# Kernel optimization log

Measured on AMD Instinct MI355X. Metric: run time of the kernel, lower is better.

## Reference

```python
import jax, jax.numpy as jnp
import numpy as np

V, E, H, L, T, B, K = 50000, 256, 512, 2, 256, 64, 32


def setup_inputs() -> dict:
    key = jax.random.key(0)
    ks = iter(jax.random.split(key, 64))
    def p(shape, scale=0.05):
        return jax.random.normal(next(ks), shape, jnp.float32) * scale
    inp = {"sentences": jax.random.randint(next(ks), (T, B), 0, V)}
    inp["emb"] = p((V, E), 0.1)
    in_sizes = [E, 2 * H]
    for l in range(L):
        for d in ("f", "r"):
            inp[f"w_ih_l{l}{d}"] = p((4 * H, in_sizes[l]))
            inp[f"w_hh_l{l}{d}"] = p((4 * H, H))
            inp[f"b_ih_l{l}{d}"] = p((4 * H,))
            inp[f"b_hh_l{l}{d}"] = p((4 * H,))
    inp["W_out"] = p((K, 2 * H))
    inp["b_out"] = p((K,))
    inp["transitions"] = p((K, K), 0.1)
    inp["start_trans"] = p((K,), 0.1)
    inp["stop_trans"] = p((K,), 0.1)
    return inp


def _lstm_dir(x, w_ih, w_hh, b_ih, b_hh, reverse):
    # x: (T, B, D). PyTorch gate order: i, f, g, o.
    Hd = w_hh.shape[1]
    xp = jnp.einsum('tbd,gd->tbg', x, w_ih) + b_ih + b_hh  # precompute input proj
    def step(carry, xt):
        h, c = carry
        g = xt + h @ w_hh.T
        i, f, gg, o = jnp.split(g, 4, axis=-1)
        c = jax.nn.sigmoid(f) * c + jax.nn.sigmoid(i) * jnp.tanh(gg)
        h = jax.nn.sigmoid(o) * jnp.tanh(c)
        return (h, c), h
    z = jnp.zeros((x.shape[1], Hd), x.dtype)
    _, hs = jax.lax.scan(step, (z, z), xp, reverse=reverse)
    return hs


def _forward(sentences, emb, layer_params, W_out, b_out, transitions, start_trans, stop_trans):
    x = emb[sentences]  # (T, B, E); dropout is identity at inference
    for (pf, pr) in layer_params:
        hf = _lstm_dir(x, *pf, reverse=False)
        hr = _lstm_dir(x, *pr, reverse=True)
        x = jnp.concatenate([hf, hr], axis=-1)  # (T, B, 2H)
    feats = jnp.einsum('tbh,kh->tbk', x, W_out) + b_out  # (T, B, K)

    # Viterbi: R[b, j, k] = transitions[j, k] + dp[b, k] + feat[b, j]
    dp0 = start_trans + feats[0]
    def vstep(dp, feat):
        R = transitions[None] + dp[:, None, :] + feat[:, :, None]
        return R.max(-1), R.argmax(-1)
    dp, bps = jax.lax.scan(vstep, dp0, feats[1:])  # bps: (T-1, B, K)
    dp = dp + stop_trans
    scores = dp.max(-1)
    last = dp.argmax(-1)
    def back(tag, bp_t):
        prev = jnp.take_along_axis(bp_t, tag[:, None], axis=1)[:, 0]
        return prev, prev
    _, pre = jax.lax.scan(back, last, bps, reverse=True)  # (T-1, B), in time order
    paths = jnp.concatenate([pre, last[None]], axis=0)  # (T, B)
    return scores, paths


def reference(sentences, emb,
              w_ih_l0f, w_hh_l0f, b_ih_l0f, b_hh_l0f,
              w_ih_l0r, w_hh_l0r, b_ih_l0r, b_hh_l0r,
              w_ih_l1f, w_hh_l1f, b_ih_l1f, b_hh_l1f,
              w_ih_l1r, w_hh_l1r, b_ih_l1r, b_hh_l1r,
              W_out, b_out, transitions, start_trans, stop_trans):
    layer_params = [
        ((w_ih_l0f, w_hh_l0f, b_ih_l0f, b_hh_l0f), (w_ih_l0r, w_hh_l0r, b_ih_l0r, b_hh_l0r)),
        ((w_ih_l1f, w_hh_l1f, b_ih_l1f, b_hh_l1f), (w_ih_l1r, w_hh_l1r, b_ih_l1r, b_hh_l1r)),
    ]
    return _forward(sentences, emb, layer_params, W_out, b_out, transitions, start_trans, stop_trans)
```

## Files before the change

### kernel.cpp

```cpp
#include <hip/hip_runtime.h>
#include <cstdint>
#include <cstddef>

#define T_ 256
#define B_ 64
#define E_ 256
#define H_ 512
#define NTAG 32
#define CHK 32
#define HSLOT 33

static constexpr size_t OX1  = 0;
static constexpr size_t SX1  = (size_t)T_*256*B_*4;
static constexpr size_t OX2  = OX1 + SX1;
static constexpr size_t SX2  = SX1;
static constexpr size_t OX0  = OX2;
static constexpr size_t OXP  = OX2 + SX2;
static constexpr size_t SXPC = (size_t)CHK*2048*B_;
static constexpr size_t SXP  = 2*SXPC;
static constexpr size_t OWHH0 = OXP + SXP;
static constexpr size_t SWHH  = (size_t)2*512*512*4;
static constexpr size_t OWHH1 = OWHH0 + SWHH;
static constexpr size_t OWIH0 = OWHH1 + SWHH;
static constexpr size_t SWIH0 = (size_t)2*2048*256;
static constexpr size_t OWIH1 = OWIH0 + SWIH0;
static constexpr size_t SWIH1 = (size_t)2*2048*1024;
static constexpr size_t OWOUT = OWIH1 + SWIH1;
static constexpr size_t SWOUT = (size_t)1024*32;
static constexpr size_t OHH   = OWOUT + SWOUT;
static constexpr size_t SHHL  = (size_t)2*HSLOT*32768;
static constexpr size_t SHH   = 2*SHHL;
static constexpr size_t OCB   = OHH + SHH;
static constexpr size_t SCB   = (size_t)2*2*512*64;
static constexpr size_t OBAR  = OCB + SCB;
static constexpr size_t SBAR  = (size_t)2*2*128*16;
static constexpr size_t OFE   = OBAR + SBAR;
static constexpr size_t SFE   = (size_t)T_*B_*NTAG;
static constexpr size_t OBP   = OFE + SFE;
static constexpr size_t SBP   = (size_t)T_*B_*NTAG/4;
static constexpr size_t WS_FLOATS = OBP + SBP;

__device__ __forceinline__ float sigf(float x){ return 1.0f/(1.0f + expf(-x)); }

__global__ void pack_whh(const float* __restrict__ w, float* __restrict__ out){
  int id = blockIdx.x*256 + threadIdx.x;
  int gate = id & 3, k = (id>>2) & 511, u = id >> 11;
  out[id] = w[((size_t)gate*512 + u)*512 + k];
}
__global__ void pack_wih(const float* __restrict__ w, float* __restrict__ out, int K, int kshift){
  int id = blockIdx.x*256 + threadIdx.x;
  int k = id & (K-1); int jj = (id>>kshift)&15; int g = id>>(kshift+4);
  out[((size_t)g*K + k)*16 + jj] = w[(size_t)(g*16+jj)*K + k];
}
__global__ void pack_wout(const float* __restrict__ w, float* __restrict__ out){
  int id = blockIdx.x*256 + threadIdx.x;
  int k = id & 1023, jj = id>>10;
  out[k*32 + jj] = w[id];
}

__global__ void gather_emb(const int* __restrict__ sent, const float* __restrict__ emb,
                           float* __restrict__ x0){
  int t = blockIdx.x; int lane = threadIdx.x & 63; int w = threadIdx.x >> 6;
  int s = sent[t*B_ + lane];
  const float4* er = (const float4*)emb + (size_t)s*(E_/4);
  float4* xo = (float4*)x0 + (size_t)t*64*64;
  #pragma unroll
  for (int q=0; q<16; ++q){
    int e4 = w*16 + q;
    xo[e4*64 + lane] = er[e4];
  }
}

__global__ __launch_bounds__(256) void proj_kernel(
    const float* __restrict__ xin, const float* __restrict__ wpack,
    const float* __restrict__ bihf, const float* __restrict__ bhhf,
    const float* __restrict__ bihr, const float* __restrict__ bhhr,
    float* __restrict__ xp, int K, int t0){
  int jg = blockIdx.x, i = blockIdx.y, dir = blockIdx.z;
  int t = dir ? (T_-1 - (t0 + i)) : (t0 + i);
  int lane = threadIdx.x & 63;
  int w = __builtin_amdgcn_readfirstlane((int)threadIdx.x) >> 6;
  int kq = K >> 2;
  int n4 = kq >> 2;
  int k40 = (w*kq) >> 2;
  const float4* xi = (const float4*)xin + (size_t)t*(K>>2)*64;
  size_t pstride = (size_t)K*16;
  const float* wp = wpack + (size_t)dir*2048*K + (size_t)(jg*2)*pstride + (size_t)w*kq*16;
  float acc[2][16];
  #pragma unroll
  for (int p=0;p<2;p++)
    #pragma unroll
    for (int jj=0;jj<16;jj++) acc[p][jj] = 0.f;
  for (int k4=0; k4<n4; ++k4){
    float4 h = xi[(k40+k4)*64 + lane];
    float hv[4] = {h.x, h.y, h.z, h.w};
    #pragma unroll
    for (int p=0;p<2;p++){
      const float* wv = wp + p*pstride + k4*64;
      #pragma unroll
      for (int ii=0;ii<4;ii++)
        #pragma unroll
        for (int jj=0;jj<16;jj++)
          acc[p][jj] = fmaf(wv[ii*16+jj], hv[ii], acc[p][jj]);
    }
  }
  __shared__ float red[4][32][64];
  #pragma unroll
  for (int p=0;p<2;p++)
    #pragma unroll
    for (int jj=0;jj<16;jj++) red[w][p*16+jj][lane] = acc[p][jj];
  __syncthreads();
  const float* b1 = dir ? bihr : bihf;
  const float* b2 = dir ? bhhr : bhhf;
  float* xpd = xp + (size_t)dir*SXPC + (size_t)i*2048*64;
  #pragma unroll
  for (int q=0;q<8;q++){
    int rr = w*8 + q;
    float v = red[0][rr][lane] + red[1][rr][lane] + red[2][rr][lane] + red[3][rr][lane];
    int row = jg*32 + rr;
    v += b1[row] + b2[row];
    xpd[(size_t)row*64 + lane] = v;
  }
}

__global__ __launch_bounds__(256,1) void rec_kernel(
    const float* __restrict__ xp, const float* __restrict__ whh,
    float* __restrict__ xout, float* __restrict__ hh, float* __restrict__ cb0,
    int* __restrict__ flags, int step0, int nsteps){
  int bid = blockIdx.x;
  int dir = bid & 1, g = bid >> 1;
  int lane = threadIdx.x & 63;
  int w = __builtin_amdgcn_readfirstlane((int)threadIdx.x >> 6);
  const float* xpd = xp + (size_t)dir*SXPC;
  const float* wbase = whh + (size_t)dir*1048576 + (size_t)g*4*2048;
  float* hhd = hh + (size_t)dir*((size_t)HSLOT*32768);
  float* cb = cb0 + dir*32768;
  int* fl = flags + dir*(128*16);
  __shared__ float red[4][16][64];
  __shared__ float hlds[256];
  int uo = g*4 + w;
  float c = cb[uo*64 + lane];
  size_t xb = ((size_t)uo)*64 + lane;
  float x0v = xpd[xb], x1v = xpd[xb+32768], x2v = xpd[xb+65536], x3v = xpd[xb+98304];
  for (int s=0; s<nsteps; ++s){
    int gstep = step0 + s;
    int t = dir ? (T_-1-gstep) : gstep;
    const float4* hp = (const float4*)(hhd + (size_t)(gstep % HSLOT)*32768);
    float4 hreg[32];
    #pragma unroll
    for (int i=0;i<32;i++) hreg[i] = hp[(w*32+i)*64 + lane];
    float acc[4][4];
    #pragma unroll
    for (int cu=0;cu<4;cu++)
      #pragma unroll
      for (int gt=0;gt<4;gt++) acc[cu][gt]=0.f;
    #pragma unroll
    for (int i=0;i<32;i++){
      float hv[4] = {hreg[i].x, hreg[i].y, hreg[i].z, hreg[i].w};
      #pragma unroll
      for (int cu=0; cu<4; cu++){
        const float4* wr = (const float4*)(wbase + (size_t)cu*2048 + (size_t)(w*128 + i*4)*4);
        #pragma unroll
        for (int kk=0;kk<4;kk++){
          float4 w4 = wr[kk];
          acc[cu][0] = fmaf(w4.x, hv[kk], acc[cu][0]);
          acc[cu][1] = fmaf(w4.y, hv[kk], acc[cu][1]);
          acc[cu][2] = fmaf(w4.z, hv[kk], acc[cu][2]);
          acc[cu][3] = fmaf(w4.w, hv[kk], acc[cu][3]);
        }
      }
    }
    #pragma unroll
    for (int cu=0;cu<4;cu++)
      #pragma unroll
      for (int gt=0;gt<4;gt++) red[w][cu*4+gt][lane] = acc[cu][gt];
    __syncthreads();
    float gv[4];
    #pragma unroll
    for (int gt=0;gt<4;gt++)
      gv[gt] = red[0][w*4+gt][lane] + red[1][w*4+gt][lane]
             + red[2][w*4+gt][lane] + red[3][w*4+gt][lane];
    gv[0] += x0v; gv[1] += x1v; gv[2] += x2v; gv[3] += x3v;
    float iv = sigf(gv[0]), fv = sigf(gv[1]);
    float gg = tanhf(gv[2]), ov = sigf(gv[3]);
    c = fv*c + iv*gg;
    float h = ov*tanhf(c);
    hlds[lane*4 + w] = h;
    __syncthreads();
    if (w == 0){
      float4 hv4 = ((const float4*)hlds)[lane];
      union { float4 f; unsigned long long q[2]; } uu; uu.f = hv4;
      unsigned long long* dst = (unsigned long long*)
          (hhd + (size_t)((gstep+1) % HSLOT)*32768 + (size_t)g*256 + (size_t)lane*4);
      __hip_atomic_store(dst+0, uu.q[0], __ATOMIC_RELAXED, __HIP_MEMORY_SCOPE_AGENT);
      __hip_atomic_store(dst+1, uu.q[1], __ATOMIC_RELAXED, __HIP_MEMORY_SCOPE_AGENT);
    } else if (w == 1){
      float4 hv4 = ((const float4*)hlds)[lane];
      float4* xo = (float4*)(xout + (size_t)t*65536 + (size_t)(dir*128 + g)*256);
      xo[lane] = hv4;
    }
    if (s < nsteps-1){
      if (w == 0){
        asm volatile("s_waitcnt vmcnt(0)" ::: "memory");
      }
      __syncthreads();
      if (threadIdx.x == 0)
        __hip_atomic_store(&fl[g*16], gstep+1, __ATOMIC_RELAXED, __HIP_MEMORY_SCOPE_AGENT);
      size_t xb2 = ((size_t)(s+1)*2048 + uo)*64 + lane;
      x0v = xpd[xb2]; x1v = xpd[xb2+32768]; x2v = xpd[xb2+65536]; x3v = xpd[xb2+98304];
      int tid = threadIdx.x;
      if (tid < 128){
        int target = gstep+1;
        int spins = 0;
        while (__hip_atomic_load(&fl[tid*16], __ATOMIC_RELAXED, __HIP_MEMORY_SCOPE_AGENT) < target){
          __builtin_amdgcn_s_sleep(1);
          if (++spins > (1<<22)) break;
        }
      }
      __syncthreads();
      asm volatile("" ::: "memory");
    }
  }
  cb[uo*64 + lane] = c;
}

__global__ __launch_bounds__(256) void feats_kernel(
    const float* __restrict__ x2, const float* __restrict__ wout,
    const float* __restrict__ bout, float* __restrict__ feats){
  int t = blockIdx.x; int lane = threadIdx.x & 63;
  int w = __builtin_amdgcn_readfirstlane((int)threadIdx.x) >> 6;
  const float4* xi = (const float4*)x2 + (size_t)t*16384;
  const float* wp = wout + (size_t)w*256*32;
  float acc[32];
  #pragma unroll
  for (int j=0;j<32;j++) acc[j] = 0.f;
  for (int k4=0;k4<64;k4++){
    float4 h = xi[(w*64 + k4)*64 + lane];
    float hv[4] = {h.x, h.y, h.z, h.w};
    const float* wv = wp + k4*128;
    #pragma unroll
    for (int ii=0;ii<4;ii++)
      #pragma unroll
      for (int j=0;j<32;j++)
        acc[j] = fmaf(wv[ii*32+j], hv[ii], acc[j]);
  }
  __shared__ float red[4][32][64];
  #pragma unroll
  for (int j=0;j<32;j++) red[w][j][lane] = acc[j];
  __syncthreads();
  __shared__ float tr[64*33];
  #pragma unroll
  for (int q=0;q<8;q++){
    int j = w*8 + q;
    float v = red[0][j][lane]+red[1][j][lane]+red[2][j][lane]+red[3][j][lane] + bout[j];
    tr[lane*33 + j] = v;
  }
  __syncthreads();
  float* fo = feats + (size_t)t*2048;
  int tid = threadIdx.x;
  #pragma unroll
  for (int q=0;q<8;q++){
    int idx = tid*8 + q;
    fo[idx] = tr[(idx>>5)*33 + (idx&31)];
  }
}

__global__ __launch_bounds__(64) void viterbi_kernel(
    const float* __restrict__ feats, const float* __restrict__ trans,
    const float* __restrict__ start, const float* __restrict__ stop,
    unsigned char* __restrict__ bp, float* __restrict__ out){
  int lane = threadIdx.x & 63;
  int b = blockIdx.x*2 + (lane>>5);
  int j = lane & 31;
  int base = lane & 32;
  float tr[32];
  #pragma unroll
  for (int k=0;k<32;k++) tr[k] = trans[j*32+k];
  float dp = start[j] + feats[b*32 + j];
  for (int t=1;t<T_;t++){
    float best = __shfl(dp, base, 64) + tr[0];
    int arg = 0;
    #pragma unroll
    for (int k=1;k<32;k++){
      float v = __shfl(dp, base + k, 64) + tr[k];
      if (v > best){ best = v; arg = k; }
    }
    dp = best + feats[((size_t)t*64 + b)*32 + j];
    bp[(size_t)(t-1)*2048 + b*32 + j] = (unsigned char)arg;
  }
  dp += stop[j];
  float bv = dp; int bi = j;
  #pragma unroll
  for (int off=1; off<32; off<<=1){
    float ov = __shfl_xor(bv, off, 64);
    int oi   = __shfl_xor(bi, off, 64);
    if (ov > bv || (ov == bv && oi < bi)){ bv = ov; bi = oi; }
  }
  if (j == 0){
    out[b] = bv;
    int cur = bi;
    out[64 + 255*64 + b] = (float)cur;
    for (int t=254;t>=0;t--){
      cur = bp[(size_t)t*2048 + b*32 + cur];
      out[64 + t*64 + b] = (float)cur;
    }
  }
}

extern "C" void kernel_launch(void* const* d_in, const int* in_sizes, int n_in,
                              void* d_out, int out_size, void* d_ws, size_t ws_size,
                              hipStream_t stream){
  const int*   sent      = (const int*)  d_in[0];
  const float* emb       = (const float*)d_in[1];
  const float* w_ih_l0f  = (const float*)d_in[2];
  const float* w_hh_l0f  = (const float*)d_in[3];
  const float* b_ih_l0f  = (const float*)d_in[4];
  const float* b_hh_l0f  = (const float*)d_in[5];
  const float* w_ih_l0r  = (const float*)d_in[6];
  const float* w_hh_l0r  = (const float*)d_in[7];
  const float* b_ih_l0r  = (const float*)d_in[8];
  const float* b_hh_l0r  = (const float*)d_in[9];
  const float* w_ih_l1f  = (const float*)d_in[10];
  const float* w_hh_l1f  = (const float*)d_in[11];
  const float* b_ih_l1f  = (const float*)d_in[12];
  const float* b_hh_l1f  = (const float*)d_in[13];
  const float* w_ih_l1r  = (const float*)d_in[14];
  const float* w_hh_l1r  = (const float*)d_in[15];
  const float* b_ih_l1r  = (const float*)d_in[16];
  const float* b_hh_l1r  = (const float*)d_in[17];
  const float* W_out     = (const float*)d_in[18];
  const float* b_out     = (const float*)d_in[19];
  const float* trans     = (const float*)d_in[20];
  const float* start_t   = (const float*)d_in[21];
  const float* stop_t    = (const float*)d_in[22];
  float* ws  = (float*)d_ws;
  float* out = (float*)d_out;

  if (ws_size < WS_FLOATS * sizeof(float)) return;

  hipMemsetAsync(ws + OHH, 0, (SHH + SCB + SBAR)*sizeof(float), stream);

  pack_whh<<<4096,256,0,stream>>>(w_hh_l0f, ws + OWHH0);
  pack_whh<<<4096,256,0,stream>>>(w_hh_l0r, ws + OWHH0 + 1048576);
  pack_whh<<<4096,256,0,stream>>>(w_hh_l1f, ws + OWHH1);
  pack_whh<<<4096,256,0,stream>>>(w_hh_l1r, ws + OWHH1 + 1048576);
  pack_wih<<<2048,256,0,stream>>>(w_ih_l0f, ws + OWIH0,           256, 8);
  pack_wih<<<2048,256,0,stream>>>(w_ih_l0r, ws + OWIH0 + 524288,  256, 8);
  pack_wih<<<8192,256,0,stream>>>(w_ih_l1f, ws + OWIH1,           1024, 10);
  pack_wih<<<8192,256,0,stream>>>(w_ih_l1r, ws + OWIH1 + 2097152, 1024, 10);
  pack_wout<<<128,256,0,stream>>>(W_out, ws + OWOUT);

  gather_emb<<<256,256,0,stream>>>(sent, emb, ws + OX0);

  const int NCH = T_ / CHK;
  dim3 gp(64, CHK, 2);
  int* bar = (int*)(ws + OBAR);

  for (int c = 0; c < NCH; ++c){
    proj_kernel<<<gp,256,0,stream>>>(ws+OX0, ws+OWIH0,
                                     b_ih_l0f,b_hh_l0f,b_ih_l0r,b_hh_l0r,
                                     ws+OXP, 256, c*CHK);
    rec_kernel<<<256,256,0,stream>>>(ws+OXP, ws+OWHH0, ws+OX1,
                                     ws+OHH, ws+OCB, bar, c*CHK, CHK);
  }
  for (int c = 0; c < NCH; ++c){
    proj_kernel<<<gp,256,0,stream>>>(ws+OX1, ws+OWIH1,
                                     b_ih_l1f,b_hh_l1f,b_ih_l1r,b_hh_l1r,
                                     ws+OXP, 1024, c*CHK);
    rec_kernel<<<256,256,0,stream>>>(ws+OXP, ws+OWHH1, ws+OX2,
                                     ws+OHH+SHHL, ws+OCB+65536,
                                     bar + 4096, c*CHK, CHK);
  }
  feats_kernel<<<256,256,0,stream>>>(ws+OX2, ws+OWOUT, b_out, ws+OFE);
  viterbi_kernel<<<32,64,0,stream>>>(ws+OFE, trans, start_t, stop_t,
                                     (unsigned char*)(ws+OBP), out);
}
```

Before: 8.943 ms.

## Split recurrent matvec across eight waves and decentralize inter-block step barrier

The recurrent LSTM kernel now runs 512 threads per block. Eight waves each reduce a 16-float4 slice of the hidden state, so the serial FMA chain per wave is halved, and four waves finish the gate math. The cross-block barrier is rewritten: the storing wave publishes its flag right after its own store drain. Each wave then polls only the 16 producer flags whose h slices it will read, which removes two block-wide __syncthreads per step. This shortens the per-step critical path, at the cost of higher register/LDS use, a larger reduction, and more complex ordering reasoning.

```diff
diff --git a/kernel.cpp b/kernel.cpp
--- a/kernel.cpp
+++ b/kernel.cpp
@@ -123,7 +123,7 @@
   }
 }
 
-__global__ __launch_bounds__(256,1) void rec_kernel(
+__global__ __launch_bounds__(512,2) void rec_kernel(
     const float* __restrict__ xp, const float* __restrict__ whh,
     float* __restrict__ xout, float* __restrict__ hh, float* __restrict__ cb0,
     int* __restrict__ flags, int step0, int nsteps){
@@ -136,30 +136,34 @@
   float* hhd = hh + (size_t)dir*((size_t)HSLOT*32768);
   float* cb = cb0 + dir*32768;
   int* fl = flags + dir*(128*16);
-  __shared__ float red[4][16][64];
+  __shared__ float red[8][16][64];
   __shared__ float hlds[256];
-  int uo = g*4 + w;
-  float c = cb[uo*64 + lane];
-  size_t xb = ((size_t)uo)*64 + lane;
-  float x0v = xpd[xb], x1v = xpd[xb+32768], x2v = xpd[xb+65536], x3v = xpd[xb+98304];
+  int uo = g*4 + (w & 3);
+  float c = 0.f;
+  float x0v = 0.f, x1v = 0.f, x2v = 0.f, x3v = 0.f;
+  if (w < 4){
+    c = cb[uo*64 + lane];
+    size_t xb = ((size_t)uo)*64 + lane;
+    x0v = xpd[xb]; x1v = xpd[xb+32768]; x2v = xpd[xb+65536]; x3v = xpd[xb+98304];
+  }
   for (int s=0; s<nsteps; ++s){
     int gstep = step0 + s;
     int t = dir ? (T_-1-gstep) : gstep;
     const float4* hp = (const float4*)(hhd + (size_t)(gstep % HSLOT)*32768);
-    float4 hreg[32];
-    #pragma unroll
-    for (int i=0;i<32;i++) hreg[i] = hp[(w*32+i)*64 + lane];
+    float4 hreg[16];
+    #pragma unroll
+    for (int i=0;i<16;i++) hreg[i] = hp[(w*16+i)*64 + lane];
     float acc[4][4];
     #pragma unroll
     for (int cu=0;cu<4;cu++)
       #pragma unroll
       for (int gt=0;gt<4;gt++) acc[cu][gt]=0.f;
     #pragma unroll
-    for (int i=0;i<32;i++){
+    for (int i=0;i<16;i++){
       float hv[4] = {hreg[i].x, hreg[i].y, hreg[i].z, hreg[i].w};
       #pragma unroll
       for (int cu=0; cu<4; cu++){
-        const float4* wr = (const float4*)(wbase + (size_t)cu*2048 + (size_t)(w*128 + i*4)*4);
+        const float4* wr = (const float4*)(wbase + (size_t)cu*2048 + (size_t)(w*64 + i*4)*4);
         #pragma unroll
         for (int kk=0;kk<4;kk++){
           float4 w4 = wr[kk];
@@ -175,53 +179,57 @@
       #pragma unroll
       for (int gt=0;gt<4;gt++) red[w][cu*4+gt][lane] = acc[cu][gt];
     __syncthreads();
-    float gv[4];
-    #pragma unroll
-    for (int gt=0;gt<4;gt++)
-      gv[gt] = red[0][w*4+gt][lane] + red[1][w*4+gt][lane]
-             + red[2][w*4+gt][lane] + red[3][w*4+gt][lane];
-    gv[0] += x0v; gv[1] += x1v; gv[2] += x2v; gv[3] += x3v;
-    float iv = sigf(gv[0]), fv = sigf(gv[1]);
-    float gg = tanhf(gv[2]), ov = sigf(gv[3]);
-    c = fv*c + iv*gg;
-    float h = ov*tanhf(c);
-    hlds[lane*4 + w] = h;
+    if (w < 4){
+      float gv[4];
+      #pragma unroll
+      for (int gt=0;gt<4;gt++){
+        float v = 0.f;
+        #pragma unroll
+        for (int w2=0;w2<8;w2++) v += red[w2][w*4+gt][lane];
+        gv[gt] = v;
+      }
+      gv[0] += x0v; gv[1] += x1v; gv[2] += x2v; gv[3] += x3v;
+      float iv = sigf(gv[0]), fv = sigf(gv[1]);
+      float gg = tanhf(gv[2]), ov = sigf(gv[3]);
+      c = fv*c + iv*gg;
+      float h = ov*tanhf(c);
+      hlds[lane*4 + w] = h;
+    }
     __syncthreads();
-    if (w == 0){
+    if (w == 4){
       float4 hv4 = ((const float4*)hlds)[lane];
       union { float4 f; unsigned long long q[2]; } uu; uu.f = hv4;
       unsigned long long* dst = (unsigned long long*)
           (hhd + (size_t)((gstep+1) % HSLOT)*32768 + (size_t)g*256 + (size_t)lane*4);
       __hip_atomic_store(dst+0, uu.q[0], __ATOMIC_RELAXED, __HIP_MEMORY_SCOPE_AGENT);
       __hip_atomic_store(dst+1, uu.q[1], __ATOMIC_RELAXED, __HIP_MEMORY_SCOPE_AGENT);
-    } else if (w == 1){
+      if (s < nsteps-1){
+        asm volatile("s_waitcnt vmcnt(0)" ::: "memory");
+        if (lane == 0)
+          __hip_atomic_store(&fl[g*16], gstep+1, __ATOMIC_RELAXED, __HIP_MEMORY_SCOPE_AGENT);
+      }
+    } else if (w == 5){
       float4 hv4 = ((const float4*)hlds)[lane];
       float4* xo = (float4*)(xout + (size_t)t*65536 + (size_t)(dir*128 + g)*256);
       xo[lane] = hv4;
     }
     if (s < nsteps-1){
-      if (w == 0){
-        asm volatile("s_waitcnt vmcnt(0)" ::: "memory");
-      }
-      __syncthreads();
-      if (threadIdx.x == 0)
-        __hip_atomic_store(&fl[g*16], gstep+1, __ATOMIC_RELAXED, __HIP_MEMORY_SCOPE_AGENT);
-      size_t xb2 = ((size_t)(s+1)*2048 + uo)*64 + lane;
-      x0v = xpd[xb2]; x1v = xpd[xb2+32768]; x2v = xpd[xb2+65536]; x3v = xpd[xb2+98304];
-      int tid = threadIdx.x;
-      if (tid < 128){
+      if (w < 4){
+        size_t xb2 = ((size_t)(s+1)*2048 + uo)*64 + lane;
+        x0v = xpd[xb2]; x1v = xpd[xb2+32768]; x2v = xpd[xb2+65536]; x3v = xpd[xb2+98304];
+      }
+      if (lane < 16){
         int target = gstep+1;
         int spins = 0;
-        while (__hip_atomic_load(&fl[tid*16], __ATOMIC_RELAXED, __HIP_MEMORY_SCOPE_AGENT) < target){
+        while (__hip_atomic_load(&fl[(w*16+lane)*16], __ATOMIC_RELAXED, __HIP_MEMORY_SCOPE_AGENT) < target){
           __builtin_amdgcn_s_sleep(1);
           if (++spins > (1<<22)) break;
         }
       }
-      __syncthreads();
       asm volatile("" ::: "memory");
     }
   }
-  cb[uo*64 + lane] = c;
+  if (w < 4) cb[uo*64 + lane] = c;
 }
 
 __global__ __launch_bounds__(256) void feats_kernel(
@@ -360,14 +368,14 @@
     proj_kernel<<<gp,256,0,stream>>>(ws+OX0, ws+OWIH0,
                                      b_ih_l0f,b_hh_l0f,b_ih_l0r,b_hh_l0r,
                                      ws+OXP, 256, c*CHK);
-    rec_kernel<<<256,256,0,stream>>>(ws+OXP, ws+OWHH0, ws+OX1,
+    rec_kernel<<<256,512,0,stream>>>(ws+OXP, ws+OWHH0, ws+OX1,
                                      ws+OHH, ws+OCB, bar, c*CHK, CHK);
   }
   for (int c = 0; c < NCH; ++c){
     proj_kernel<<<gp,256,0,stream>>>(ws+OX1, ws+OWIH1,
                                      b_ih_l1f,b_hh_l1f,b_ih_l1r,b_hh_l1r,
                                      ws+OXP, 1024, c*CHK);
-    rec_kernel<<<256,256,0,stream>>>(ws+OXP, ws+OWHH1, ws+OX2,
+    rec_kernel<<<256,512,0,stream>>>(ws+OXP, ws+OWHH1, ws+OX2,
                                      ws+OHH+SHHL, ws+OCB+65536,
                                      bar + 4096, c*CHK, CHK);
   }
```

New measurement: 9.324 ms. 1.04x slower.

## Split recurrent LSTM step into batch-tile groups with per-group barriers

Applied to the files above, without the earlier changes.

Restructures the persistent recurrent kernel so that each group of 32 blocks handles one direction and a 16-column batch tile. Grid-wide synchronisation becomes per-group flag barriers over 32 blocks instead of 128. Blocks now use 512 threads: the hidden state is staged into LDS and a k-split is reduced with cross-lane shuffles rather than an LDS reduction. W_hh is repacked so each block reads weights for unit pairs. This aims to shrink barrier fan-in and latency per timestep, at the cost of each block re-reading its weight slice for every batch tile.

```diff
diff --git a/kernel.cpp b/kernel.cpp
--- a/kernel.cpp
+++ b/kernel.cpp
@@ -28,12 +28,12 @@
 static constexpr size_t OWOUT = OWIH1 + SWIH1;
 static constexpr size_t SWOUT = (size_t)1024*32;
 static constexpr size_t OHH   = OWOUT + SWOUT;
-static constexpr size_t SHHL  = (size_t)2*HSLOT*32768;
+static constexpr size_t SHHL  = (size_t)8*HSLOT*8192;
 static constexpr size_t SHH   = 2*SHHL;
 static constexpr size_t OCB   = OHH + SHH;
-static constexpr size_t SCB   = (size_t)2*2*512*64;
+static constexpr size_t SCB   = (size_t)2*8*8192;
 static constexpr size_t OBAR  = OCB + SCB;
-static constexpr size_t SBAR  = (size_t)2*2*128*16;
+static constexpr size_t SBAR  = (size_t)2*8*32*16;
 static constexpr size_t OFE   = OBAR + SBAR;
 static constexpr size_t SFE   = (size_t)T_*B_*NTAG;
 static constexpr size_t OBP   = OFE + SFE;
@@ -42,9 +42,10 @@
 
 __device__ __forceinline__ float sigf(float x){ return 1.0f/(1.0f + expf(-x)); }
 
-__global__ void pack_whh(const float* __restrict__ w, float* __restrict__ out){
+__global__ void pack_whh2(const float* __restrict__ w, float* __restrict__ out){
   int id = blockIdx.x*256 + threadIdx.x;
-  int gate = id & 3, k = (id>>2) & 511, u = id >> 11;
+  int jj = id & 7, k = (id>>3) & 511, upair = id >> 12;
+  int u = upair*2 + (jj>>2), gate = jj & 3;
   out[id] = w[((size_t)gate*512 + u)*512 + k];
 }
 __global__ void pack_wih(const float* __restrict__ w, float* __restrict__ out, int K, int kshift){
@@ -123,105 +124,109 @@
   }
 }
 
-__global__ __launch_bounds__(256,1) void rec_kernel(
+__global__ __launch_bounds__(512,2) void rec_kernel(
     const float* __restrict__ xp, const float* __restrict__ whh,
     float* __restrict__ xout, float* __restrict__ hh, float* __restrict__ cb0,
     int* __restrict__ flags, int step0, int nsteps){
   int bid = blockIdx.x;
-  int dir = bid & 1, g = bid >> 1;
-  int lane = threadIdx.x & 63;
-  int w = __builtin_amdgcn_readfirstlane((int)threadIdx.x >> 6);
+  int g = bid & 7;
+  int m = bid >> 3;
+  int dir = g & 1, bt = g >> 1;
+  int tid = threadIdx.x;
+  int lane = tid & 63;
+  int w = __builtin_amdgcn_readfirstlane(tid >> 6);
+  int bl = lane & 15, kq = lane >> 4;
+  int bglobal = bt*16 + bl;
+  int u0 = m*16 + w*2;
+  int upair = u0 >> 1;
   const float* xpd = xp + (size_t)dir*SXPC;
-  const float* wbase = whh + (size_t)dir*1048576 + (size_t)g*4*2048;
-  float* hhd = hh + (size_t)dir*((size_t)HSLOT*32768);
-  float* cb = cb0 + dir*32768;
-  int* fl = flags + dir*(128*16);
-  __shared__ float red[4][16][64];
-  __shared__ float hlds[256];
-  int uo = g*4 + w;
-  float c = cb[uo*64 + lane];
-  size_t xb = ((size_t)uo)*64 + lane;
-  float x0v = xpd[xb], x1v = xpd[xb+32768], x2v = xpd[xb+65536], x3v = xpd[xb+98304];
+  const float4* wp4 = (const float4*)(whh + (size_t)dir*1048576)
+                      + (size_t)upair*1024 + (size_t)kq*256;
+  float* hhd = hh + (size_t)g*((size_t)HSLOT*8192);
+  float* cbg = cb0 + (size_t)g*8192;
+  int* fl = flags + g*512;
+  __shared__ float4 hlds[2048];
+  float c0 = cbg[upair*32 + bl*2 + 0];
+  float c1 = cbg[upair*32 + bl*2 + 1];
+  int k4o = m*4 + (w>>1);
+  int inner = (w&1)*2;
   for (int s=0; s<nsteps; ++s){
     int gstep = step0 + s;
     int t = dir ? (T_-1-gstep) : gstep;
-    const float4* hp = (const float4*)(hhd + (size_t)(gstep % HSLOT)*32768);
-    float4 hreg[32];
-    #pragma unroll
-    for (int i=0;i<32;i++) hreg[i] = hp[(w*32+i)*64 + lane];
-    float acc[4][4];
-    #pragma unroll
-    for (int cu=0;cu<4;cu++)
+    float xpv[8];
+    #pragma unroll
+    for (int g4=0; g4<4; ++g4){
+      xpv[g4*2+0] = xpd[(size_t)s*131072 + (size_t)(g4*512 + u0    )*64 + bglobal];
+      xpv[g4*2+1] = xpd[(size_t)s*131072 + (size_t)(g4*512 + u0 + 1)*64 + bglobal];
+    }
+    if (s > 0 && lane < 4){
+      int target = gstep;
+      int spins = 0;
+      while (__hip_atomic_load(&fl[(w*4+lane)*16], __ATOMIC_RELAXED, __HIP_MEMORY_SCOPE_AGENT) < target){
+        __builtin_amdgcn_s_sleep(1);
+        if (++spins > (1<<22)) break;
+      }
+    }
+    asm volatile("" ::: "memory");
+    const float4* hsrc = (const float4*)hhd + (size_t)(gstep % HSLOT)*2048;
+    #pragma unroll
+    for (int j=0;j<4;++j)
+      hlds[w*256 + j*64 + lane] = hsrc[w*256 + j*64 + lane];
+    __syncthreads();
+    float acc[8];
+    #pragma unroll
+    for (int a=0;a<8;a++) acc[a]=0.f;
+    int hb = kq*512 + bl;
+    for (int c4=0; c4<32; ++c4){
+      float4 h4 = hlds[hb + c4*16];
+      float hk[4] = {h4.x, h4.y, h4.z, h4.w};
       #pragma unroll
-      for (int gt=0;gt<4;gt++) acc[cu][gt]=0.f;
-    #pragma unroll
-    for (int i=0;i<32;i++){
-      float hv[4] = {hreg[i].x, hreg[i].y, hreg[i].z, hreg[i].w};
-      #pragma unroll
-      for (int cu=0; cu<4; cu++){
-        const float4* wr = (const float4*)(wbase + (size_t)cu*2048 + (size_t)(w*128 + i*4)*4);
-        #pragma unroll
-        for (int kk=0;kk<4;kk++){
-          float4 w4 = wr[kk];
-          acc[cu][0] = fmaf(w4.x, hv[kk], acc[cu][0]);
-          acc[cu][1] = fmaf(w4.y, hv[kk], acc[cu][1]);
-          acc[cu][2] = fmaf(w4.z, hv[kk], acc[cu][2]);
-          acc[cu][3] = fmaf(w4.w, hv[kk], acc[cu][3]);
-        }
+      for (int kk=0; kk<4; ++kk){
+        float4 wa = wp4[(c4*4+kk)*2 + 0];
+        float4 wb = wp4[(c4*4+kk)*2 + 1];
+        acc[0] = fmaf(wa.x, hk[kk], acc[0]);
+        acc[1] = fmaf(wa.y, hk[kk], acc[1]);
+        acc[2] = fmaf(wa.z, hk[kk], acc[2]);
+        acc[3] = fmaf(wa.w, hk[kk], acc[3]);
+        acc[4] = fmaf(wb.x, hk[kk], acc[4]);
+        acc[5] = fmaf(wb.y, hk[kk], acc[5]);
+        acc[6] = fmaf(wb.z, hk[kk], acc[6]);
+        acc[7] = fmaf(wb.w, hk[kk], acc[7]);
       }
     }
     #pragma unroll
-    for (int cu=0;cu<4;cu++)
-      #pragma unroll
-      for (int gt=0;gt<4;gt++) red[w][cu*4+gt][lane] = acc[cu][gt];
-    __syncthreads();
-    float gv[4];
-    #pragma unroll
-    for (int gt=0;gt<4;gt++)
-      gv[gt] = red[0][w*4+gt][lane] + red[1][w*4+gt][lane]
-             + red[2][w*4+gt][lane] + red[3][w*4+gt][lane];
-    gv[0] += x0v; gv[1] += x1v; gv[2] += x2v; gv[3] += x3v;
-    float iv = sigf(gv[0]), fv = sigf(gv[1]);
-    float gg = tanhf(gv[2]), ov = sigf(gv[3]);
-    c = fv*c + iv*gg;
-    float h = ov*tanhf(c);
-    hlds[lane*4 + w] = h;
-    __syncthreads();
-    if (w == 0){
-      float4 hv4 = ((const float4*)hlds)[lane];
-      union { float4 f; unsigned long long q[2]; } uu; uu.f = hv4;
+    for (int a=0;a<8;a++){
+      acc[a] += __shfl_xor(acc[a], 16, 64);
+      acc[a] += __shfl_xor(acc[a], 32, 64);
+    }
+    float i0 = sigf(acc[0] + xpv[0]), f0 = sigf(acc[1] + xpv[2]);
+    float g0 = tanhf(acc[2] + xpv[4]), o0 = sigf(acc[3] + xpv[6]);
+    c0 = f0*c0 + i0*g0;
+    float h0 = o0*tanhf(c0);
+    float i1 = sigf(acc[4] + xpv[1]), f1 = sigf(acc[5] + xpv[3]);
+    float g1 = tanhf(acc[6] + xpv[5]), o1 = sigf(acc[7] + xpv[7]);
+    c1 = f1*c1 + i1*g1;
+    float h1 = o1*tanhf(c1);
+    if (kq == 0){
+      union { float f[2]; unsigned long long q; } uu;
+      uu.f[0] = h0; uu.f[1] = h1;
       unsigned long long* dst = (unsigned long long*)
-          (hhd + (size_t)((gstep+1) % HSLOT)*32768 + (size_t)g*256 + (size_t)lane*4);
-      __hip_atomic_store(dst+0, uu.q[0], __ATOMIC_RELAXED, __HIP_MEMORY_SCOPE_AGENT);
-      __hip_atomic_store(dst+1, uu.q[1], __ATOMIC_RELAXED, __HIP_MEMORY_SCOPE_AGENT);
-    } else if (w == 1){
-      float4 hv4 = ((const float4*)hlds)[lane];
-      float4* xo = (float4*)(xout + (size_t)t*65536 + (size_t)(dir*128 + g)*256);
-      xo[lane] = hv4;
+          (hhd + (size_t)((gstep+1) % HSLOT)*8192 + (size_t)(k4o*16 + bl)*4 + inner);
+      __hip_atomic_store(dst, uu.q, __ATOMIC_RELAXED, __HIP_MEMORY_SCOPE_AGENT);
+      float2 hv2; hv2.x = h0; hv2.y = h1;
+      *(float2*)(xout + ((size_t)t*16384 + (size_t)(dir*128 + k4o)*64 + bglobal)*4 + inner) = hv2;
     }
     if (s < nsteps-1){
-      if (w == 0){
-        asm volatile("s_waitcnt vmcnt(0)" ::: "memory");
-      }
+      asm volatile("s_waitcnt vmcnt(0)" ::: "memory");
       __syncthreads();
-      if (threadIdx.x == 0)
-        __hip_atomic_store(&fl[g*16], gstep+1, __ATOMIC_RELAXED, __HIP_MEMORY_SCOPE_AGENT);
-      size_t xb2 = ((size_t)(s+1)*2048 + uo)*64 + lane;
-      x0v = xpd[xb2]; x1v = xpd[xb2+32768]; x2v = xpd[xb2+65536]; x3v = xpd[xb2+98304];
-      int tid = threadIdx.x;
-      if (tid < 128){
-        int target = gstep+1;
-        int spins = 0;
-        while (__hip_atomic_load(&fl[tid*16], __ATOMIC_RELAXED, __HIP_MEMORY_SCOPE_AGENT) < target){
-          __builtin_amdgcn_s_sleep(1);
-          if (++spins > (1<<22)) break;
-        }
-      }
-      __syncthreads();
-      asm volatile("" ::: "memory");
-    }
-  }
-  cb[uo*64 + lane] = c;
+      if (tid == 0)
+        __hip_atomic_store(&fl[m*16], gstep+1, __ATOMIC_RELAXED, __HIP_MEMORY_SCOPE_AGENT);
+    }
+  }
+  if (kq == 0){
+    float2 cv; cv.x = c0; cv.y = c1;
+    *(float2*)(cbg + upair*32 + bl*2) = cv;
+  }
 }
 
 __global__ __launch_bounds__(256) void feats_kernel(
@@ -340,10 +345,10 @@
 
   hipMemsetAsync(ws + OHH, 0, (SHH + SCB + SBAR)*sizeof(float), stream);
 
-  pack_whh<<<4096,256,0,stream>>>(w_hh_l0f, ws + OWHH0);
-  pack_whh<<<4096,256,0,stream>>>(w_hh_l0r, ws + OWHH0 + 1048576);
-  pack_whh<<<4096,256,0,stream>>>(w_hh_l1f, ws + OWHH1);
-  pack_whh<<<4096,256,0,stream>>>(w_hh_l1r, ws + OWHH1 + 1048576);
+  pack_whh2<<<4096,256,0,stream>>>(w_hh_l0f, ws + OWHH0);
+  pack_whh2<<<4096,256,0,stream>>>(w_hh_l0r, ws + OWHH0 + 1048576);
+  pack_whh2<<<4096,256,0,stream>>>(w_hh_l1f, ws + OWHH1);
+  pack_whh2<<<4096,256,0,stream>>>(w_hh_l1r, ws + OWHH1 + 1048576);
   pack_wih<<<2048,256,0,stream>>>(w_ih_l0f, ws + OWIH0,           256, 8);
   pack_wih<<<2048,256,0,stream>>>(w_ih_l0r, ws + OWIH0 + 524288,  256, 8);
   pack_wih<<<8192,256,0,stream>>>(w_ih_l1f, ws + OWIH1,           1024, 10);
@@ -360,14 +365,14 @@
     proj_kernel<<<gp,256,0,stream>>>(ws+OX0, ws+OWIH0,
                                      b_ih_l0f,b_hh_l0f,b_ih_l0r,b_hh_l0r,
                                      ws+OXP, 256, c*CHK);
-    rec_kernel<<<256,256,0,stream>>>(ws+OXP, ws+OWHH0, ws+OX1,
+    rec_kernel<<<256,512,0,stream>>>(ws+OXP, ws+OWHH0, ws+OX1,
                                      ws+OHH, ws+OCB, bar, c*CHK, CHK);
   }
   for (int c = 0; c < NCH; ++c){
     proj_kernel<<<gp,256,0,stream>>>(ws+OX1, ws+OWIH1,
                                      b_ih_l1f,b_hh_l1f,b_ih_l1r,b_hh_l1r,
                                      ws+OXP, 1024, c*CHK);
-    rec_kernel<<<256,256,0,stream>>>(ws+OXP, ws+OWHH1, ws+OX2,
+    rec_kernel<<<256,512,0,stream>>>(ws+OXP, ws+OWHH1, ws+OX2,
                                      ws+OHH+SHHL, ws+OCB+65536,
                                      bar + 4096, c*CHK, CHK);
   }
```

Result: slower. 11.79 ms (+31.8%).

## Replace all-to-all flag polling with aggregator blocks broadcasting epoch counters

Applied to the files above, without the earlier changes.

Adds 8 aggregator blocks to the recurrent kernel, four per direction. Each one polls all 128 per-block step flags of its direction and then publishes a single epoch counter. Compute blocks now spin on one shard's epoch word with a single thread, instead of 128 threads each polling every flag. This cuts contention on the flag cache lines in the global barrier but adds a relay hop of latency per step. It relies on all 264 blocks being co-resident, and it lowers the spin timeout.

```diff
diff --git a/kernel.cpp b/kernel.cpp
--- a/kernel.cpp
+++ b/kernel.cpp
@@ -9,6 +9,7 @@
 #define NTAG 32
 #define CHK 32
 #define HSLOT 33
+#define SPIN_MAX (1<<18)
 
 static constexpr size_t OX1  = 0;
 static constexpr size_t SX1  = (size_t)T_*256*B_*4;
@@ -38,6 +39,7 @@
 static constexpr size_t SFE   = (size_t)T_*B_*NTAG;
 static constexpr size_t OBP   = OFE + SFE;
 static constexpr size_t SBP   = (size_t)T_*B_*NTAG/4;
+static constexpr size_t OEP   = OBP + 130560;
 static constexpr size_t WS_FLOATS = OBP + SBP;
 
 __device__ __forceinline__ float sigf(float x){ return 1.0f/(1.0f + expf(-x)); }
@@ -126,9 +128,28 @@
 __global__ __launch_bounds__(256,1) void rec_kernel(
     const float* __restrict__ xp, const float* __restrict__ whh,
     float* __restrict__ xout, float* __restrict__ hh, float* __restrict__ cb0,
-    int* __restrict__ flags, int step0, int nsteps){
+    int* __restrict__ flags, int* __restrict__ ep, int step0, int nsteps){
   int bid = blockIdx.x;
-  int dir = bid & 1, g = bid >> 1;
+  if (bid < 8){
+    int a = bid;
+    int* afl = flags + (a&1)*(128*16);
+    for (int s2=1; s2<nsteps; ++s2){
+      int target = step0 + s2;
+      if (threadIdx.x < 128){
+        int spins = 0;
+        while (__hip_atomic_load(&afl[threadIdx.x*16], __ATOMIC_RELAXED, __HIP_MEMORY_SCOPE_AGENT) < target){
+          __builtin_amdgcn_s_sleep(1);
+          if (++spins > SPIN_MAX) break;
+        }
+      }
+      __syncthreads();
+      if (threadIdx.x == 0)
+        __hip_atomic_store(&ep[a*16], target, __ATOMIC_RELAXED, __HIP_MEMORY_SCOPE_AGENT);
+    }
+    return;
+  }
+  int cbid = bid - 8;
+  int dir = cbid & 1, g = cbid >> 1;
   int lane = threadIdx.x & 63;
   int w = __builtin_amdgcn_readfirstlane((int)threadIdx.x >> 6);
   const float* xpd = xp + (size_t)dir*SXPC;
@@ -136,6 +157,7 @@
   float* hhd = hh + (size_t)dir*((size_t)HSLOT*32768);
   float* cb = cb0 + dir*32768;
   int* fl = flags + dir*(128*16);
+  int shard = dir + 2*((cbid>>3)&3);
   __shared__ float red[4][16][64];
   __shared__ float hlds[256];
   int uo = g*4 + w;
@@ -208,13 +230,12 @@
         __hip_atomic_store(&fl[g*16], gstep+1, __ATOMIC_RELAXED, __HIP_MEMORY_SCOPE_AGENT);
       size_t xb2 = ((size_t)(s+1)*2048 + uo)*64 + lane;
       x0v = xpd[xb2]; x1v = xpd[xb2+32768]; x2v = xpd[xb2+65536]; x3v = xpd[xb2+98304];
-      int tid = threadIdx.x;
-      if (tid < 128){
+      if (threadIdx.x == 0){
         int target = gstep+1;
         int spins = 0;
-        while (__hip_atomic_load(&fl[tid*16], __ATOMIC_RELAXED, __HIP_MEMORY_SCOPE_AGENT) < target){
+        while (__hip_atomic_load(&ep[shard*16], __ATOMIC_RELAXED, __HIP_MEMORY_SCOPE_AGENT) < target){
           __builtin_amdgcn_s_sleep(1);
-          if (++spins > (1<<22)) break;
+          if (++spins > SPIN_MAX) break;
         }
       }
       __syncthreads();
@@ -339,6 +360,7 @@
   if (ws_size < WS_FLOATS * sizeof(float)) return;
 
   hipMemsetAsync(ws + OHH, 0, (SHH + SCB + SBAR)*sizeof(float), stream);
+  hipMemsetAsync(ws + OEP, 0, 512*sizeof(float), stream);
 
   pack_whh<<<4096,256,0,stream>>>(w_hh_l0f, ws + OWHH0);
   pack_whh<<<4096,256,0,stream>>>(w_hh_l0r, ws + OWHH0 + 1048576);
@@ -355,21 +377,23 @@
   const int NCH = T_ / CHK;
   dim3 gp(64, CHK, 2);
   int* bar = (int*)(ws + OBAR);
+  int* ep0 = (int*)(ws + OEP);
+  int* ep1 = ep0 + 128;
 
   for (int c = 0; c < NCH; ++c){
     proj_kernel<<<gp,256,0,stream>>>(ws+OX0, ws+OWIH0,
                                      b_ih_l0f,b_hh_l0f,b_ih_l0r,b_hh_l0r,
                                      ws+OXP, 256, c*CHK);
-    rec_kernel<<<256,256,0,stream>>>(ws+OXP, ws+OWHH0, ws+OX1,
-                                     ws+OHH, ws+OCB, bar, c*CHK, CHK);
+    rec_kernel<<<264,256,0,stream>>>(ws+OXP, ws+OWHH0, ws+OX1,
+                                     ws+OHH, ws+OCB, bar, ep0, c*CHK, CHK);
   }
   for (int c = 0; c < NCH; ++c){
     proj_kernel<<<gp,256,0,stream>>>(ws+OX1, ws+OWIH1,
                                      b_ih_l1f,b_hh_l1f,b_ih_l1r,b_hh_l1r,
                                      ws+OXP, 1024, c*CHK);
-    rec_kernel<<<256,256,0,stream>>>(ws+OXP, ws+OWHH1, ws+OX2,
+    rec_kernel<<<264,256,0,stream>>>(ws+OXP, ws+OWHH1, ws+OX2,
                                      ws+OHH+SHHL, ws+OCB+65536,
-                                     bar + 4096, c*CHK, CHK);
+                                     bar + 4096, ep1, c*CHK, CHK);
   }
   feats_kernel<<<256,256,0,stream>>>(ws+OX2, ws+OWOUT, b_out, ws+OFE);
   viterbi_kernel<<<32,64,0,stream>>>(ws+OFE, trans, start_t, stop_t,
```

Result: slower. 9.162 ms (+2.5%).
